# Kernel tuning notes

Measured on AMD Instinct MI355X. Metric: run time of the kernel, lower is better.

The kernel has to match this reference:

```python
import jax, jax.numpy as jnp
import numpy as np
from jax import lax


def _compute_Bp(lam):
    # Bʹ[k, j] = 1 / prod_{i != j} (1 - λ_i / λ_j), via log-sum for stability.
    k, n = lam.shape
    ratios = lam[:, :, None] / lam[:, None, :]           # [k, n, n], entry (i, j) = λ_i / λ_j
    eye = jnp.eye(n, dtype=bool)[None]                    # zero out diagonal (log(1-0)=0)
    ratios = jnp.where(eye, jnp.zeros((), ratios.dtype), ratios)
    lnBp = -jnp.sum(jnp.log(1.0 - ratios), axis=1)        # [k, n]
    return jnp.exp(lnBp)


def _linear_recurrence(a, b):
    # s_t = a_t * s_{t-1} + b_t (elementwise, diagonal), parallel associative scan over time.
    def combine(c1, c2):
        a1, b1 = c1
        a2, b2 = c2
        return a1 * a2, b1 * a2 + b2
    return lax.associative_scan(combine, (a, b), axis=0)[1]


def _ldstack_forward(x, R, theta, lnC_r, lnC_i, D, Do):
    b, T, d = x.shape
    k, half_n = theta.shape
    n = 2 * half_n
    m = D.shape[1]

    # average=True path: project d -> k, go time-major, lift to complex
    xp = jnp.einsum('btd,dk->btk', x, R)
    xc = jnp.transpose(xp, (1, 0, 2)).astype(jnp.complex64)      # [T, b, k]

    # unitary_constitute: λ = exp(i * [θ, -θ]) on the unit circle
    lam = jnp.exp(jnp.concatenate([theta, -theta], axis=1) * 1j)  # [k, n] complex64
    Cp = jnp.exp(lnC_r + 1j * lnC_i)                              # [k, n, m] complex64

    Bp = _compute_Bp(lam)                                         # [k, n]
    Bx = xc[..., None] * Bp                                       # [T, b, k, n]
    al = jnp.broadcast_to(lam, (T, b, k, n))                      # α is None for Δ=1

    # standard=True: shift coefficients one step (state lags input)
    zeros = jnp.zeros((1, b, k, n), dtype=jnp.complex64)
    al = jnp.concatenate([zeros, al[:-1]], axis=0)
    Bx = jnp.concatenate([zeros, Bx[:-1]], axis=0)

    s = _linear_recurrence(al, Bx)                                # [T, b, k, n]

    Cs = jnp.einsum('tbkn,knm->tbkm', s, Cp)                      # readout
    Dx = xc[..., None] * D.astype(jnp.complex64)[None, None]      # [T, b, k, m]
    y = Cs + Dx + Do.astype(jnp.complex64)                        # [T, b, k, m]

    y = jnp.mean(y, axis=2)                                       # average over k
    y = jnp.real(y)                                               # [T, b, m]
    return jnp.transpose(y, (1, 0, 2))                            # [b, T, m]


def setup_inputs() -> dict:
    b, T, d = 8, 2048, 128
    k, n, m = 32, 32, 128
    key = jax.random.key(0)
    ks = jax.random.split(key, 7)
    x = jax.random.normal(ks[0], (b, T, d), dtype=jnp.float32)
    R = jax.random.normal(ks[1], (d, k), dtype=jnp.float32)
    theta = jax.random.uniform(ks[2], (k, n // 2), dtype=jnp.float32,
                               minval=-np.pi, maxval=np.pi)
    lnC_r = 1e-4 * jax.random.normal(ks[3], (k, n, m), dtype=jnp.float32)
    lnC_i = 1e-4 * jax.random.normal(ks[4], (k, n, m), dtype=jnp.float32)
    D = jax.random.uniform(ks[5], (k, m), dtype=jnp.float32, minval=-1e-3, maxval=1e-3)
    Do = jax.random.uniform(ks[6], (m,), dtype=jnp.float32, minval=-1e-7, maxval=1e-7)
    return {"x": x, "R": R, "theta": theta, "lnC_r": lnC_r, "lnC_i": lnC_i,
            "D": D, "Do": Do}


def reference(x, R, theta, lnC_r, lnC_i, D, Do):
    return _ldstack_forward(x, R, theta, lnC_r, lnC_i, D, Do)
```

## Files before the change

kernel.cpp:

```cpp
#include <hip/hip_runtime.h>
#include <hip/hip_bf16.h>
#include <math.h>

#define K_  32
#define HN  16
#define N_  32
#define M_  128
#define B_  8
#define T_  2048
#define D_  128
#define BT  (B_*T_)
#define KA  1056
#define CHK 32
#define CL  64
#define ABYTES 2176

typedef short short8 __attribute__((ext_vector_type(8)));
typedef float floatx4 __attribute__((ext_vector_type(4)));
typedef unsigned short ushort_t;
typedef unsigned int uint_t;

__device__ __forceinline__ ushort_t f2bf(float f) {
    __hip_bfloat16 h = __float2bfloat16(f);
    return *reinterpret_cast<ushort_t*>(&h);
}
__device__ __forceinline__ uint_t pack_bf2(float re, float im) {
    return ((uint_t)f2bf(im) << 16) | (uint_t)f2bf(re);
}

__global__ __launch_bounds__(256) void k_pre(const float* __restrict__ theta,
                                             const float* __restrict__ lnC_r,
                                             const float* __restrict__ lnC_i,
                                             const float* __restrict__ D,
                                             const float* __restrict__ x,
                                             const float* __restrict__ R,
                                             float* __restrict__ ws,
                                             ushort_t* __restrict__ Wt,
                                             float* __restrict__ xpT,
                                             ushort_t* __restrict__ A2) {
    __shared__ float xls[32 * 128];
    int bid = blockIdx.x, tid = threadIdx.x;
    if (bid == 0) {
        #pragma unroll
        for (int rep = 0; rep < 2; ++rep) {
            int t2 = rep * 256 + tid;
            int k = t2 >> 4, j = t2 & 15;
            float angj = theta[k * HN + j];
            float pr = 1.f, pi = 0.f;
            for (int i = 0; i < N_; ++i) {
                if (i == j) continue;
                float angi = (i < HN) ? theta[k * HN + i] : -theta[k * HN + i - HN];
                float d = angi - angj;
                float tr = 1.f - cosf(d);
                float ti = -sinf(d);
                float nr = pr * tr - pi * ti;
                float ni = pr * ti + pi * tr;
                pr = nr; pi = ni;
            }
            float den = pr * pr + pi * pi;
            ws[t2]        = cosf(angj);
            ws[512 + t2]  = sinf(angj);
            ws[1024 + t2] = pr / den;
            ws[1536 + t2] = -pi / den;
        }
    } else if (bid <= 272) {
        int t = (bid - 1) * 256 + tid;
        const float inv = 1.f / 32.f;
        if (t < K_ * HN * M_) {
            int m = t & 127, j = (t >> 7) & 15, k = t >> 11;
            int i0 = (k * N_ + j) * M_ + m;
            int i1 = (k * N_ + j + HN) * M_ + m;
            float r0 = expf(lnC_r[i0]), c0 = cosf(lnC_i[i0]), s0 = sinf(lnC_i[i0]);
            float r1 = expf(lnC_r[i1]), c1 = cosf(lnC_i[i1]), s1 = sinf(lnC_i[i1]);
            float wr = (r0 * c0 + r1 * c1) * inv;
            float wi = (r1 * s1 - r0 * s0) * inv;
            *(uint_t*)(Wt + (size_t)m * KA + k * 32 + 2 * j) = pack_bf2(wr, wi);
        } else if (t < K_ * HN * M_ + K_ * M_) {
            int u = t - K_ * HN * M_;
            int m = u & 127, k = u >> 7;
            Wt[(size_t)m * KA + 1024 + k] = f2bf(D[k * M_ + m] * inv);
        }
    } else {
        int xb = bid - 273;
        int b = xb >> 6;
        int tbase = (xb & 63) * 32;
        const float4* xsrc = (const float4*)(x + ((size_t)b * T_ + tbase) * D_);
        float4* xd = (float4*)xls;
        #pragma unroll
        for (int e = 0; e < 4; ++e) xd[tid + 256 * e] = xsrc[tid + 256 * e];
        __syncthreads();
        int kk = tid & 31, rg = tid >> 5;
        float accv[4] = {0.f, 0.f, 0.f, 0.f};
        #pragma unroll 4
        for (int i = 0; i < D_; ++i) {
            float rv = R[i * K_ + kk];
            #pragma unroll
            for (int rr = 0; rr < 4; ++rr)
                accv[rr] += xls[(rg + 8 * rr) * D_ + i] * rv;
        }
        #pragma unroll
        for (int rr = 0; rr < 4; ++rr) {
            int tt = tbase + rg + 8 * rr;
            A2[(size_t)(tt * 8 + b) * KA + 1024 + kk] = f2bf(accv[rr]);
            size_t base = (size_t)(b * K_ + kk) * T_;
            if (tt < T_ - 1) xpT[base + tt + 1] = accv[rr];
            if (tt == 0)     xpT[base] = 0.f;
        }
    }
}

__global__ __launch_bounds__(512) void k_scan(const float* __restrict__ xpT,
                                              const float* __restrict__ ws,
                                              uint_t* __restrict__ A2u) {
    __shared__ float xls[T_];
    __shared__ float Er[512], Ei[512];

    int tid = threadIdx.x;
    int k = blockIdx.x & 31, b = blockIdx.x >> 5;
    int c = tid >> 4, j = tid & 15;
    int col = k * 16 + j;

    ((float4*)xls)[tid] = ((const float4*)(xpT + (size_t)(b * K_ + k) * T_))[tid];
    __syncthreads();

    float lr = ws[col], li = ws[512 + col];
    float br = ws[1024 + col], bi = ws[1536 + col];

    {
        float sr = 0.f, si = 0.f;
        const float* xc = xls + c * CL;
        #pragma unroll 4
        for (int p = 0; p < CL; ++p) {
            float x1 = xc[p];
            float nr = br * x1 + lr * sr - li * si;
            float ni = bi * x1 + lr * si + li * sr;
            sr = nr; si = ni;
        }
        Er[c * 16 + j] = sr;
        Ei[c * 16 + j] = si;
    }
    __syncthreads();

    if (tid < 16) {
        float pr = lr, pi = li;
        #pragma unroll
        for (int q = 0; q < 6; ++q) {
            float nr = pr * pr - pi * pi;
            float ni = 2.f * pr * pi;
            pr = nr; pi = ni;
        }
        float sr = 0.f, si = 0.f;
        for (int cc = 0; cc < CHK; ++cc) {
            int idx = cc * 16 + tid;
            float er = Er[idx], ei = Ei[idx];
            Er[idx] = sr; Ei[idx] = si;
            float nr = pr * sr - pi * si + er;
            float ni = pr * si + pi * sr + ei;
            sr = nr; si = ni;
        }
    }
    __syncthreads();

    {
        float sr = Er[c * 16 + j], si = Ei[c * 16 + j];
        int t0 = c * CL;
        const float* xc = xls + t0;
        uint_t* Ab = A2u + (size_t)(t0 * 8 + b) * (KA / 2) + col;
        #pragma unroll 4
        for (int p = 0; p < CL; ++p) {
            float x1 = xc[p];
            float nr = br * x1 + lr * sr - li * si;
            float ni = bi * x1 + lr * si + li * sr;
            sr = nr; si = ni;
            Ab[0] = pack_bf2(sr, si);
            Ab += 8 * (KA / 2);
        }
    }
}

__global__ __launch_bounds__(512) void k_gemm2(const uint_t* __restrict__ A2u,
                                               const ushort_t* __restrict__ Wt,
                                               const float* __restrict__ Do,
                                               float* __restrict__ out) {
    __shared__ __align__(16) char smem[32 * ABYTES];

    int tid = threadIdx.x;
    int bid = blockIdx.x;

    const uint_t* src = A2u + (size_t)bid * (32 * (KA / 2));
    for (int it = 0; it < 33; ++it) {
        int f = it * 512 + tid;
        int row = f / 528;
        int uc = f - row * 528;
        int bo = (row * ABYTES + uc * 4) ^ ((row & 7) << 4);
        *(uint_t*)(smem + bo) = src[f];
    }
    __syncthreads();

    int wave = tid >> 6, lane = tid & 63;
    int l16 = lane & 15, quad = lane >> 4;
    int rh = wave & 1, cf = wave >> 1;
    int arow = rh * 16 + l16;
    int abase = arow * ABYTES + quad * 16;
    int aswz = (arow & 7) << 4;
    const ushort_t* Wp0 = Wt + (size_t)(cf * 32 + l16) * KA + quad * 8;
    const ushort_t* Wp1 = Wp0 + (size_t)16 * KA;

    floatx4 acc0 = {0.f, 0.f, 0.f, 0.f}, acc1 = {0.f, 0.f, 0.f, 0.f};
    for (int ks = 0; ks < 33; ++ks) {
        short8 av = *(const short8*)(smem + ((abase + ks * 64) ^ aswz));
        short8 b0 = *(const short8*)(Wp0 + ks * 32);
        short8 b1 = *(const short8*)(Wp1 + ks * 32);
        acc0 = __builtin_amdgcn_mfma_f32_16x16x32_bf16(av, b0, acc0, 0, 0, 0);
        acc1 = __builtin_amdgcn_mfma_f32_16x16x32_bf16(av, b1, acc1, 0, 0, 0);
    }

    int col0 = cf * 32 + l16;
    float dv0 = Do[col0], dv1 = Do[col0 + 16];
    #pragma unroll
    for (int q = 0; q < 4; ++q) {
        int r = bid * 32 + rh * 16 + quad * 4 + q;
        int b = r & 7, t = r >> 3;
        float* op = out + (size_t)(b * T_ + t) * M_;
        op[col0]      = acc0[q] + dv0;
        op[col0 + 16] = acc1[q] + dv1;
    }
}

extern "C" void kernel_launch(void* const* d_in, const int* in_sizes, int n_in,
                              void* d_out, int out_size, void* d_ws, size_t ws_size,
                              hipStream_t stream) {
    const float* x     = (const float*)d_in[0];
    const float* R     = (const float*)d_in[1];
    const float* theta = (const float*)d_in[2];
    const float* lnC_r = (const float*)d_in[3];
    const float* lnC_i = (const float*)d_in[4];
    const float* D     = (const float*)d_in[5];
    const float* Do    = (const float*)d_in[6];
    float* out = (float*)d_out;

    float* wsf   = (float*)d_ws;
    float* lambp = wsf;
    ushort_t* Wt = (ushort_t*)(wsf + 2048);
    ushort_t* A2 = (ushort_t*)(wsf + 2048 + 67584);
    float* xpT   = wsf + 2048 + 67584 + 8650752;

    k_pre<<<785, 256, 0, stream>>>(theta, lnC_r, lnC_i, D, x, R,
                                   lambp, Wt, xpT, A2);
    k_scan<<<256, 512, 0, stream>>>(xpT, lambp, (uint_t*)A2);
    k_gemm2<<<512, 512, 0, stream>>>((const uint_t*)A2, Wt, Do, out);
}
```

Baseline: 126.9 us.

## Split scan into seed kernel and separate coalesced expansion kernel

The scan kernel no longer writes the full state sequence. It only computes chunk-boundary seeds at 32-step granularity and stores them. A new expand kernel with 512 blocks, one per (batch, 32-step chunk), reruns the short recurrence from each seed and writes the bf16 states with every row written fully by one block. This is meant to improve parallelism and write coalescing for the state writes, at the cost of an extra launch, recomputing the recurrence, and a seed buffer round trip.

```diff
diff --git a/kernel.cpp b/kernel.cpp
--- a/kernel.cpp
+++ b/kernel.cpp
@@ -109,9 +109,9 @@
     }
 }
 
-__global__ __launch_bounds__(512) void k_scan(const float* __restrict__ xpT,
+__global__ __launch_bounds__(512) void k_seed(const float* __restrict__ xpT,
                                               const float* __restrict__ ws,
-                                              uint_t* __restrict__ A2u) {
+                                              float2* __restrict__ seeds) {
     __shared__ float xls[T_];
     __shared__ float Er[512], Ei[512];
 
@@ -163,18 +163,49 @@
 
     {
         float sr = Er[c * 16 + j], si = Ei[c * 16 + j];
-        int t0 = c * CL;
-        const float* xc = xls + t0;
-        uint_t* Ab = A2u + (size_t)(t0 * 8 + b) * (KA / 2) + col;
+        size_t sb = ((size_t)(b * 64 + 2 * c) * 512) + col;
+        seeds[sb] = make_float2(sr, si);
+        const float* xc = xls + c * CL;
         #pragma unroll 4
-        for (int p = 0; p < CL; ++p) {
+        for (int p = 0; p < 32; ++p) {
             float x1 = xc[p];
             float nr = br * x1 + lr * sr - li * si;
             float ni = bi * x1 + lr * si + li * sr;
             sr = nr; si = ni;
-            Ab[0] = pack_bf2(sr, si);
-            Ab += 8 * (KA / 2);
-        }
+        }
+        seeds[sb + 512] = make_float2(sr, si);
+    }
+}
+
+__global__ __launch_bounds__(512) void k_expand(const float* __restrict__ xpT,
+                                                const float* __restrict__ ws,
+                                                const float2* __restrict__ seeds,
+                                                uint_t* __restrict__ A2u) {
+    __shared__ float xs[32 * 33];
+    int tid = threadIdx.x;
+    int b = blockIdx.x >> 6, c32 = blockIdx.x & 63;
+    int t0 = c32 * 32;
+    int k = tid >> 4, j = tid & 15;
+
+    {
+        const float* src = xpT + (size_t)(b * K_ + k) * T_ + t0;
+        for (int p = j; p < 32; p += 16) xs[k * 33 + p] = src[p];
+    }
+    float lr = ws[tid], li = ws[512 + tid];
+    float br = ws[1024 + tid], bi = ws[1536 + tid];
+    float2 sd = seeds[((size_t)(b * 64 + c32) * 512) + tid];
+    __syncthreads();
+
+    float sr = sd.x, si = sd.y;
+    uint_t* Ab = A2u + (size_t)(t0 * 8 + b) * (KA / 2) + tid;
+    #pragma unroll 4
+    for (int p = 0; p < 32; ++p) {
+        float x1 = xs[k * 33 + p];
+        float nr = br * x1 + lr * sr - li * si;
+        float ni = bi * x1 + lr * si + li * sr;
+        sr = nr; si = ni;
+        Ab[0] = pack_bf2(sr, si);
+        Ab += 8 * (KA / 2);
     }
 }
 
@@ -239,14 +270,16 @@
     const float* Do    = (const float*)d_in[6];
     float* out = (float*)d_out;
 
-    float* wsf   = (float*)d_ws;
-    float* lambp = wsf;
-    ushort_t* Wt = (ushort_t*)(wsf + 2048);
-    ushort_t* A2 = (ushort_t*)(wsf + 2048 + 67584);
-    float* xpT   = wsf + 2048 + 67584 + 8650752;
+    float* wsf    = (float*)d_ws;
+    float* lambp  = wsf;
+    ushort_t* Wt  = (ushort_t*)(wsf + 2048);
+    ushort_t* A2  = (ushort_t*)(wsf + 2048 + 67584);
+    float* xpT    = wsf + 2048 + 67584 + 8650752;
+    float2* seeds = (float2*)(wsf + 2048 + 67584 + 8650752 + 524288);
 
     k_pre<<<785, 256, 0, stream>>>(theta, lnC_r, lnC_i, D, x, R,
                                    lambp, Wt, xpT, A2);
-    k_scan<<<256, 512, 0, stream>>>(xpT, lambp, (uint_t*)A2);
+    k_seed<<<256, 512, 0, stream>>>(xpT, lambp, seeds);
+    k_expand<<<512, 512, 0, stream>>>(xpT, lambp, seeds, (uint_t*)A2);
     k_gemm2<<<512, 512, 0, stream>>>((const uint_t*)A2, Wt, Do, out);
 }
```

Measured after the change: 129.5 us. 2.1% more time.
